# Performance work log

Hardware: AMD Instinct MI355X
Metric: run time of the kernel (lower is better)

The kernel has to match this reference:

```python
import jax, jax.numpy as jnp
import numpy as np

EPS = 1e-5
D = 4  # max_displacement


def _conv(x, w, b, stride, pad):
    # x: [B,C,H,W], w: [O,I,kh,kw]
    y = jax.lax.conv_general_dilated(x, w, (stride, stride), [(pad, pad), (pad, pad)],
                                     dimension_numbers=('NCHW', 'OIHW', 'NCHW'))
    return y + b[None, :, None, None]


def _bn(x, g, b, m, v):
    # eval-mode batchnorm with running stats
    scale = (g * jax.lax.rsqrt(v + EPS))[None, :, None, None]
    return (x - m[None, :, None, None]) * scale + b[None, :, None, None]


def _extract(x, w1, b1, g1, be1, m1, v1, w2, b2, g2, be2, m2, v2, w3, b3, g3, be3, m3, v3):
    x = jax.nn.relu(_bn(_conv(x, w1, b1, 2, 3), g1, be1, m1, v1))
    x = jax.nn.relu(_bn(_conv(x, w2, b2, 2, 1), g2, be2, m2, v2))
    x = jax.nn.relu(_bn(_conv(x, w3, b3, 2, 1), g3, be3, m3, v3))
    return x  # [B,256,H/8,W/8]


def _correlation(x1, x2):
    # shifted-window correlation, 81 shifts (structural loop, static slices)
    B, C, H, W = x1.shape
    x2p = jnp.pad(x2, ((0, 0), (0, 0), (D, D), (D, D)))
    maps = [jnp.sum(x1 * x2p[:, :, i:i + H, j:j + W], axis=1)
            for i in range(2 * D + 1) for j in range(2 * D + 1)]
    return jnp.stack(maps, axis=1)  # [B,81,H,W]


def _gmm(cloth_img, person_img, fe, fw1, fb1, fw2, fb2, fw3, fb3):
    cf = _extract(cloth_img, *fe)
    pf = _extract(person_img, *fe)
    corr = _correlation(cf, pf)
    x = jax.nn.relu(_conv(corr, fw1, fb1, 1, 1))
    x = jax.nn.relu(_conv(x, fw2, fb2, 1, 1))
    return _conv(x, fw3, fb3, 1, 1)  # [B,2,H/8,W/8]


def setup_inputs() -> dict:
    key = jax.random.key(0)
    ks = jax.random.split(key, 32)
    B, H, W = 8, 512, 512
    w = lambda k, shape, s=0.05: jax.random.normal(k, shape, jnp.float32) * s
    inp = {}
    inp['cloth_img'] = jax.random.normal(ks[0], (B, 3, H, W), jnp.float32)
    inp['person_img'] = jax.random.normal(ks[1], (B, 3, H, W), jnp.float32)
    inp['w1'] = w(ks[2], (64, 3, 7, 7)); inp['b1'] = w(ks[3], (64,))
    inp['g1'] = 1.0 + w(ks[4], (64,)); inp['be1'] = w(ks[5], (64,))
    inp['m1'] = w(ks[6], (64,)); inp['v1'] = jax.random.uniform(ks[7], (64,), jnp.float32, 0.5, 1.5)
    inp['w2'] = w(ks[8], (128, 64, 3, 3)); inp['b2'] = w(ks[9], (128,))
    inp['g2'] = 1.0 + w(ks[10], (128,)); inp['be2'] = w(ks[11], (128,))
    inp['m2'] = w(ks[12], (128,)); inp['v2'] = jax.random.uniform(ks[13], (128,), jnp.float32, 0.5, 1.5)
    inp['w3'] = w(ks[14], (256, 128, 3, 3)); inp['b3'] = w(ks[15], (256,))
    inp['g3'] = 1.0 + w(ks[16], (256,)); inp['be3'] = w(ks[17], (256,))
    inp['m3'] = w(ks[18], (256,)); inp['v3'] = jax.random.uniform(ks[19], (256,), jnp.float32, 0.5, 1.5)
    inp['fw1'] = w(ks[20], (128, 81, 3, 3)); inp['fb1'] = w(ks[21], (128,))
    inp['fw2'] = w(ks[22], (64, 128, 3, 3)); inp['fb2'] = w(ks[23], (64,))
    inp['fw3'] = w(ks[24], (2, 64, 3, 3)); inp['fb3'] = w(ks[25], (2,))
    return inp


def reference(cloth_img, person_img,
              w1, b1, g1, be1, m1, v1,
              w2, b2, g2, be2, m2, v2,
              w3, b3, g3, be3, m3, v3,
              fw1, fb1, fw2, fb2, fw3, fb3):
    fe = (w1, b1, g1, be1, m1, v1, w2, b2, g2, be2, m2, v2, w3, b3, g3, be3, m3, v3)
    return _gmm(cloth_img, person_img, fe, fw1, fb1, fw2, fb2, fw3, fb3)
```

## Files before the change

### kernel.cpp

```cpp
#include <hip/hip_runtime.h>

typedef __bf16 bf16x8_t __attribute__((ext_vector_type(8)));
typedef float f32x4 __attribute__((ext_vector_type(4)));
typedef unsigned short u16x8 __attribute__((ext_vector_type(8)));
typedef unsigned short u16x4 __attribute__((ext_vector_type(4)));

#define EPS 1e-5f

__device__ __forceinline__ unsigned short f2bf(float f) {
    unsigned u = __builtin_bit_cast(unsigned, f);
    u += 0x7fff + ((u >> 16) & 1);
    return (unsigned short)(u >> 16);
}

__device__ __forceinline__ void gload16(const unsigned short* g, unsigned short* l) {
    __builtin_amdgcn_global_load_lds(
        (const __attribute__((address_space(1))) unsigned int*)g,
        (__attribute__((address_space(3))) unsigned int*)l,
        16, 0, 0);
}

template <int N> __device__ __forceinline__ void s_waitcnt_vm() {
    if constexpr (N == 0)       asm volatile("s_waitcnt vmcnt(0)" ::: "memory");
    else if constexpr (N == 8)  asm volatile("s_waitcnt vmcnt(8)" ::: "memory");
    else if constexpr (N == 10) asm volatile("s_waitcnt vmcnt(10)" ::: "memory");
    else if constexpr (N == 12) asm volatile("s_waitcnt vmcnt(12)" ::: "memory");
    else static_assert(N == 0, "unsupported vmcnt");
}

__global__ void prep_affine_all(const float* __restrict__ b1, const float* __restrict__ g1,
                                const float* __restrict__ be1, const float* __restrict__ m1,
                                const float* __restrict__ v1,
                                const float* __restrict__ b2, const float* __restrict__ g2,
                                const float* __restrict__ be2, const float* __restrict__ m2,
                                const float* __restrict__ v2,
                                const float* __restrict__ b3, const float* __restrict__ g3,
                                const float* __restrict__ be3, const float* __restrict__ m3,
                                const float* __restrict__ v3,
                                const float* __restrict__ fb1, const float* __restrict__ fb2,
                                const float* __restrict__ fb3, float* __restrict__ aff) {
    int i = blockIdx.x * 256 + threadIdx.x;
    if (i < 64) {
        float s = g1[i] * rsqrtf(v1[i] + EPS);
        aff[i] = s; aff[64 + i] = (b1[i] - m1[i]) * s + be1[i];
    } else if (i < 192) {
        int c = i - 64; float s = g2[c] * rsqrtf(v2[c] + EPS);
        aff[128 + c] = s; aff[256 + c] = (b2[c] - m2[c]) * s + be2[c];
    } else if (i < 448) {
        int c = i - 192; float s = g3[c] * rsqrtf(v3[c] + EPS);
        aff[384 + c] = s; aff[640 + c] = (b3[c] - m3[c]) * s + be3[c];
    } else if (i < 576) {
        int c = i - 448; aff[896 + c] = 1.f; aff[1024 + c] = fb1[c];
    } else if (i < 640) {
        int c = i - 576; aff[1152 + c] = 1.f; aff[1216 + c] = fb2[c];
    } else if (i < 642) {
        int c = i - 640; aff[1280 + c] = 1.f; aff[1288 + c] = fb3[c];
    }
}

__device__ __forceinline__ void wconv3x3(const float* __restrict__ w, unsigned short* __restrict__ dst,
                                         int Cout, int Sp, int Kp, int CIN, int CINP, int idx) {
    if (idx >= Sp * Kp) return;
    int m = idx / Kp, k = idx - m * Kp;
    int tap = k / CINP, ic = k - tap * CINP;
    unsigned short v = 0;
    if (m < Cout && tap < 9 && ic < CIN) {
        int kh = tap / 3, kw = tap - kh * 3;
        v = f2bf(w[((m * CIN + ic) * 3 + kh) * 3 + kw]);
    }
    dst[idx] = v;
}

__global__ void conv_weights_all(const float* __restrict__ w1, const float* __restrict__ w2,
                                 const float* __restrict__ w3, const float* __restrict__ fw1,
                                 const float* __restrict__ fw2, const float* __restrict__ fw3,
                                 unsigned short* d1, unsigned short* d2, unsigned short* d3,
                                 unsigned short* d4, unsigned short* d5, unsigned short* d6) {
    int idx = blockIdx.x * 256 + threadIdx.x;
    switch (blockIdx.y) {
    case 0: {
        if (idx >= 64 * 256) return;
        int m = idx >> 8, k = idx & 255;
        int kh = k >> 5, r = k & 31, kw = r >> 2, ic = r & 3;
        unsigned short v = 0;
        if (kh < 7 && kw < 7 && ic < 3) v = f2bf(w1[((m * 3 + ic) * 7 + kh) * 7 + kw]);
        d1[idx] = v;
    } break;
    case 1: wconv3x3(w2, d2, 128, 128, 576, 64, 64, idx); break;
    case 2: wconv3x3(w3, d3, 256, 256, 1152, 128, 128, idx); break;
    case 3: wconv3x3(fw1, d4, 128, 128, 1152, 81, 128, idx); break;
    case 4: wconv3x3(fw2, d5, 64, 64, 1152, 128, 128, idx); break;
    case 5: wconv3x3(fw3, d6, 2, 64, 576, 64, 64, idx); break;
    }
}

__global__ void to_nhwc4(const float* __restrict__ cloth, const float* __restrict__ person,
                         unsigned short* __restrict__ dst) {
    int z = blockIdx.z;
    const float* src = (z < 8) ? cloth + (size_t)z * 786432
                               : person + (size_t)(z - 8) * 786432;
    int p = blockIdx.x * 256 + threadIdx.x;
    int row = p >> 9, col = p & 511;
    u16x4 o;
    o[0] = f2bf(src[p]);
    o[1] = f2bf(src[262144 + p]);
    o[2] = f2bf(src[524288 + p]);
    o[3] = 0;
    *(u16x4*)&dst[(size_t)z * 1073296 + ((size_t)(row + 3) * 518 + col + 3) * 4] = o;
}

__global__ void ring3_zero(unsigned short* __restrict__ buf) {
    int z = blockIdx.y;
    int p = blockIdx.x * 256 + threadIdx.x;
    if (p >= 6180) return;
    int r, c;
    if (p < 1554) { r = p / 518; c = p - (p / 518) * 518; }
    else if (p < 3108) { int q = p - 1554; r = 515 + q / 518; c = q - (q / 518) * 518; }
    else { int q = p - 3108; r = 3 + q / 6; int k = q - (q / 6) * 6; c = (k < 3) ? k : 512 + k; }
    const u16x4 zv = {0, 0, 0, 0};
    *(u16x4*)&buf[(size_t)z * 1073296 + ((size_t)r * 518 + c) * 4] = zv;
}

__global__ void border_zero(unsigned short* __restrict__ buf, int Hp, int Wp, int C8,
                            int imgStrideElems, int nimg) {
    int idx = blockIdx.x * 256 + threadIdx.x;
    int nb = 2 * Wp + 2 * (Hp - 2);
    int per = nb * C8;
    if (idx >= per * nimg) return;
    int z = idx / per, q = idx - z * per;
    int p = q / C8, cc = q - p * C8;
    int row, col;
    if (p < Wp) { row = 0; col = p; }
    else if (p < 2 * Wp) { row = Hp - 1; col = p - Wp; }
    else { int e = p - 2 * Wp; row = 1 + (e >> 1); col = (e & 1) ? Wp - 1 : 0; }
    const u16x8 zv = {0, 0, 0, 0, 0, 0, 0, 0};
    *(u16x8*)&buf[(size_t)z * imgStrideElems + ((size_t)row * Wp + col) * (C8 * 8) + cc * 8] = zv;
}

template <int WR, int WS, int MODE, bool RELU, bool OUT_NCHW, int CIN, int NKT,
          int HIN, int WOS, int STRIDE, int OPAD, int PIPE>
__global__ __launch_bounds__(WR * WS * 64)
void gemm_conv(const unsigned short* __restrict__ X, const unsigned short* __restrict__ Wmk,
               const float* __restrict__ scale, const float* __restrict__ shift,
               void* __restrict__ Yv, int Cout, int xImgStride, int yImgStride) {
    constexpr int BR = WR * 64, BS = WS * 64, NT = WR * WS * 64;
    constexpr int SXC = BR * 8 / NT, SWC = BS * 8 / NT;
    constexpr int NLOAD = SXC + SWC;
    constexpr int KP = (MODE == 1) ? NKT * 64 : 256;
    constexpr int WP = HIN + ((MODE == 2) ? 6 : 2);
    constexpr int WOUT = 1 << WOS;
    constexpr int WOP = WOUT + 2 * OPAD;
    constexpr int NBUF = PIPE ? 2 : 1;
    constexpr int EPS_LDK = BS + 8;
    constexpr int GEMM_ELEMS = NBUF * (BR + BS) * 64;
    constexpr int EPI_ELEMS = BR * EPS_LDK;
    constexpr int LDS_ELEMS = GEMM_ELEMS > EPI_ELEMS ? GEMM_ELEMS : EPI_ELEMS;
    __shared__ __align__(16) unsigned short lds[LDS_ELEMS];
    unsigned short* XsB = lds;
    unsigned short* WsB = lds + NBUF * BR * 64;
    const int tid = threadIdx.x;
    const int lane = tid & 63, wid = tid >> 6;
    const int wr = wid % WR, wsx = wid / WR;
    int bx = blockIdx.x;
    { const int nx = gridDim.x; bx = (bx & 7) * (nx >> 3) + (bx >> 3); }
    const int r0 = bx * BR, s0 = blockIdx.y * BS;
    const int z = blockIdx.z;
    const int lr = lane & 15, lk = lane >> 4;
    const unsigned short* Ximg = X + (size_t)z * xImgStride;

    const unsigned short* xsrc[SXC];
    #pragma unroll
    for (int i = 0; i < SXC; ++i) {
        int c = i * NT + tid;
        int row = c >> 3, chs = (c & 7) ^ (row & 7);
        int r = r0 + row;
        int oh = r >> WOS, ow = r & (WOUT - 1);
        if (MODE == 1)
            xsrc[i] = Ximg + ((size_t)(oh * STRIDE) * WP + (size_t)(ow * STRIDE)) * CIN + chs * 8;
        else
            xsrc[i] = Ximg + ((size_t)(2 * oh + (chs >> 2)) * WP + 2 * ow + (chs & 3) * 2) * 4;
    }
    const unsigned short* wsrc[SWC];
    #pragma unroll
    for (int i = 0; i < SWC; ++i) {
        int c = i * NT + tid;
        int row = c >> 3, chs = (c & 7) ^ (row & 7);
        wsrc[i] = Wmk + (size_t)(s0 + row) * KP + chs * 8;
    }

    int arow[4], brow[4];
    #pragma unroll
    for (int mi = 0; mi < 4; ++mi) arow[mi] = (wr * 64 + mi * 16 + lr) * 64;
    #pragma unroll
    for (int si = 0; si < 4; ++si) brow[si] = (wsx * 64 + si * 16 + lr) * 64;

    const f32x4 fz = {0.f, 0.f, 0.f, 0.f};
    f32x4 acc[4][4];
    #pragma unroll
    for (int a = 0; a < 4; ++a)
        #pragma unroll
        for (int b = 0; b < 4; ++b) acc[a][b] = fz;

    auto stage = [&](int kt, int b) {
        size_t koff;
        if (MODE == 1) {
            const int tap = (kt * 64) / CIN;
            const int kh = tap / 3, kw = tap - (tap / 3) * 3;
            const int icb0 = (kt * 64) % CIN;
            koff = ((size_t)kh * WP + kw) * CIN + icb0;
        } else {
            koff = (size_t)kt * 2 * WP * 4;
        }
        #pragma unroll
        for (int i = 0; i < SXC; ++i)
            gload16(xsrc[i] + koff, &XsB[b * BR * 64 + (i * NT + wid * 64) * 8]);
        #pragma unroll
        for (int i = 0; i < SWC; ++i)
            gload16(wsrc[i] + (size_t)kt * 64, &WsB[b * BS * 64 + (i * NT + wid * 64) * 8]);
    };
    auto compute = [&](int b) {
        #pragma unroll
        for (int hf = 0; hf < 2; ++hf) {
            const int cA = (((hf * 4 + lk) ^ (lr & 7)) * 8);
            u16x8 af[4], bfr[4];
            #pragma unroll
            for (int mi = 0; mi < 4; ++mi) af[mi] = *(const u16x8*)&XsB[b * BR * 64 + arow[mi] + cA];
            #pragma unroll
            for (int si = 0; si < 4; ++si) bfr[si] = *(const u16x8*)&WsB[b * BS * 64 + brow[si] + cA];
            #pragma unroll
            for (int mi = 0; mi < 4; ++mi)
                #pragma unroll
                for (int si = 0; si < 4; ++si)
                    acc[mi][si] = __builtin_amdgcn_mfma_f32_16x16x32_bf16(
                        __builtin_bit_cast(bf16x8_t, af[mi]),
                        __builtin_bit_cast(bf16x8_t, bfr[si]), acc[mi][si], 0, 0, 0);
        }
    };

    if (PIPE == 0) {
        #pragma unroll
        for (int kt = 0; kt < NKT; ++kt) {
            stage(kt, 0);
            __syncthreads();
            compute(0);
            __syncthreads();
        }
    } else {
        stage(0, 0);
        #pragma unroll
        for (int kt = 0; kt < NKT; ++kt) {
            const int cur = kt & 1;
            if (kt + 1 < NKT) {
                stage(kt + 1, cur ^ 1);
                s_waitcnt_vm<NLOAD>();
            } else {
                s_waitcnt_vm<0>();
            }
            __builtin_amdgcn_sched_barrier(0);
            __builtin_amdgcn_s_barrier();
            __builtin_amdgcn_sched_barrier(0);
            compute(cur);
            __builtin_amdgcn_sched_barrier(0);
            __builtin_amdgcn_s_barrier();
        }
    }

    if (OUT_NCHW) {
        #pragma unroll
        for (int si = 0; si < 4; ++si) {
            int col = s0 + wsx * 64 + si * 16 + lr;
            bool cok = col < Cout;
            float sc = cok ? scale[col] : 0.f;
            float sh = cok ? shift[col] : 0.f;
            #pragma unroll
            for (int mi = 0; mi < 4; ++mi) {
                int rbase = r0 + wr * 64 + mi * 16 + lk * 4;
                #pragma unroll
                for (int j = 0; j < 4; ++j) {
                    float v = acc[mi][si][j] * sc + sh;
                    if (RELU) v = fmaxf(v, 0.f);
                    if (cok) ((float*)Yv)[(size_t)z * yImgStride + col * 4096 + rbase + j] = v;
                }
            }
        }
    } else {
        __syncthreads();
        unsigned short* epi = lds;
        #pragma unroll
        for (int si = 0; si < 4; ++si) {
            int col = wsx * 64 + si * 16 + lr;
            float sc = scale[s0 + col];
            float sh = shift[s0 + col];
            #pragma unroll
            for (int mi = 0; mi < 4; ++mi) {
                int rowl = wr * 64 + mi * 16 + lk * 4;
                #pragma unroll
                for (int j = 0; j < 4; ++j) {
                    float v = acc[mi][si][j] * sc + sh;
                    if (RELU) v = fmaxf(v, 0.f);
                    epi[(rowl + j) * EPS_LDK + col] = f2bf(v);
                }
            }
        }
        __syncthreads();
        constexpr int NCH = BR * BS / 8 / NT;
        constexpr int CPR = BS / 8;
        #pragma unroll
        for (int i = 0; i < NCH; ++i) {
            int c = i * NT + tid;
            int row = c / CPR, colc = c - (c / CPR) * CPR;
            int r = r0 + row;
            int oh = r >> WOS, ow = r & (WOUT - 1);
            size_t off = ((size_t)(oh + OPAD) * WOP + ow + OPAD) * Cout + s0 + colc * 8;
            *(u16x8*)((unsigned short*)Yv + (size_t)z * yImgStride + off) =
                *(const u16x8*)&epi[row * EPS_LDK + colc * 8];
        }
    }
}

__global__ __launch_bounds__(256)
void corr_mfma(const unsigned short* __restrict__ cf,
               const unsigned short* __restrict__ pf,
               unsigned short* __restrict__ out) {
    const int h = blockIdx.x;
    const int z = blockIdx.y;
    const int tid = threadIdx.x;
    const int lane = tid & 63, t = tid >> 6;
    const int lr = lane & 15, lk = lane >> 4;
    const unsigned short* cfi = cf + (size_t)z * 1048576;
    const unsigned short* pfi = pf + (size_t)z * 1048576;
    unsigned short* outp = out + (size_t)z * 557568;

    u16x8 a[8];
    {
        const unsigned short* ap = cfi + ((size_t)(h * 64 + t * 16 + lr)) * 256 + lk * 8;
        #pragma unroll
        for (int ks = 0; ks < 8; ++ks) a[ks] = *(const u16x8*)(ap + ks * 32);
    }

    const u16x8 zz = {0, 0, 0, 0, 0, 0, 0, 0};
    for (int di = -4; di <= 4; ++di) {
        const int h2 = h + di;
        const bool hok = (unsigned)h2 < 64u;
        #pragma unroll
        for (int ct = 0; ct < 2; ++ct) {
            const int wpg = t * 16 - 8 + ct * 16 + lr;
            u16x8 b[8];
            if (hok && (unsigned)wpg < 64u) {
                const unsigned short* bp = pfi + ((size_t)(h2 * 64 + wpg)) * 256 + lk * 8;
                #pragma unroll
                for (int ks = 0; ks < 8; ++ks) b[ks] = *(const u16x8*)(bp + ks * 32);
            } else {
                #pragma unroll
                for (int ks = 0; ks < 8; ++ks) b[ks] = zz;
            }
            f32x4 acc0 = {0.f, 0.f, 0.f, 0.f}, acc1 = {0.f, 0.f, 0.f, 0.f};
            #pragma unroll
            for (int ks = 0; ks < 8; ks += 2) {
                acc0 = __builtin_amdgcn_mfma_f32_16x16x32_bf16(
                    __builtin_bit_cast(bf16x8_t, a[ks]),
                    __builtin_bit_cast(bf16x8_t, b[ks]), acc0, 0, 0, 0);
                acc1 = __builtin_amdgcn_mfma_f32_16x16x32_bf16(
                    __builtin_bit_cast(bf16x8_t, a[ks + 1]),
                    __builtin_bit_cast(bf16x8_t, b[ks + 1]), acc1, 0, 0, 0);
            }
            const int wl = lk * 4;
            const int wpl = ct * 16 - 8 + lr;
            #pragma unroll
            for (int j = 0; j < 4; ++j) {
                int dj = wpl - (wl + j);
                if (dj >= -4 && dj <= 4) {
                    int s = (di + 4) * 9 + dj + 4;
                    int w = t * 16 + wl + j;
                    outp[((size_t)(h + 1) * 66 + w + 1) * 128 + s] =
                        f2bf(acc0[j] + acc1[j]);
                }
            }
        }
    }
}

extern "C" void kernel_launch(void* const* d_in, const int* in_sizes, int n_in,
                              void* d_out, int out_size, void* d_ws, size_t ws_size,
                              hipStream_t stream) {
    const float* cloth  = (const float*)d_in[0];
    const float* person = (const float*)d_in[1];
    const float* w1 = (const float*)d_in[2];  const float* b1 = (const float*)d_in[3];
    const float* g1 = (const float*)d_in[4];  const float* be1 = (const float*)d_in[5];
    const float* m1 = (const float*)d_in[6];  const float* v1 = (const float*)d_in[7];
    const float* w2 = (const float*)d_in[8];  const float* b2 = (const float*)d_in[9];
    const float* g2 = (const float*)d_in[10]; const float* be2 = (const float*)d_in[11];
    const float* m2 = (const float*)d_in[12]; const float* v2 = (const float*)d_in[13];
    const float* w3 = (const float*)d_in[14]; const float* b3 = (const float*)d_in[15];
    const float* g3 = (const float*)d_in[16]; const float* be3 = (const float*)d_in[17];
    const float* m3 = (const float*)d_in[18]; const float* v3 = (const float*)d_in[19];
    const float* fw1 = (const float*)d_in[20]; const float* fb1 = (const float*)d_in[21];
    const float* fw2 = (const float*)d_in[22]; const float* fb2 = (const float*)d_in[23];
    const float* fw3 = (const float*)d_in[24]; const float* fb3 = (const float*)d_in[25];

    char* ws = (char*)d_ws;
    auto U = [&](size_t off) { return (unsigned short*)(ws + off); };
    unsigned short* nhwc = U(0);
    unsigned short* t1   = U(34345472);
    unsigned short* cf   = U(34345472);
    unsigned short* t2   = U(170668544);
    unsigned short* w1mk  = U(239890944);
    unsigned short* w2mk  = U(239923712);
    unsigned short* w3mk  = U(240071168);
    unsigned short* fw1mk = U(240660992);
    unsigned short* fw2mk = U(240955904);
    unsigned short* fw3mk = U(241103360);
    float* aff = (float*)(ws + 241177088);
    unsigned short* corr = U(241185280);
    unsigned short* f1b  = U(250106368);
    unsigned short* f2b  = U(259027456);
    float *s1 = aff,         *sh1 = aff + 64,   *s2 = aff + 128,  *sh2 = aff + 256;
    float *s3 = aff + 384,   *sh3 = aff + 640,  *sf1 = aff + 896, *shf1 = aff + 1024;
    float *sf2 = aff + 1152, *shf2 = aff + 1216, *sf3 = aff + 1280, *shf3 = aff + 1288;

    prep_affine_all<<<3, 256, 0, stream>>>(b1, g1, be1, m1, v1, b2, g2, be2, m2, v2,
                                           b3, g3, be3, m3, v3, fb1, fb2, fb3, aff);
    conv_weights_all<<<dim3(1152, 6), 256, 0, stream>>>(w1, w2, w3, fw1, fw2, fw3,
                                                        w1mk, w2mk, w3mk, fw1mk, fw2mk, fw3mk);

    ring3_zero<<<dim3(25, 16), 256, 0, stream>>>(nhwc);
    hipMemsetAsync(ws + 241185280, 0, 22302720, stream);
    border_zero<<<514, 256, 0, stream>>>(t1, 258, 258, 8, 4260096, 16);
    border_zero<<<517, 256, 0, stream>>>(t2, 130, 130, 16, 2163200, 16);

    to_nhwc4<<<dim3(1024, 1, 16), 256, 0, stream>>>(cloth, person, nhwc);

    gemm_conv<4, 1, 2, true, false, 4, 4, 512, 8, 2, 1, 0><<<dim3(256, 1, 16), 256, 0, stream>>>(
        nhwc, w1mk, s1, sh1, t1, 64, 1073296, 4260096);
    gemm_conv<2, 2, 1, true, false, 64, 9, 256, 7, 2, 1, 1><<<dim3(128, 1, 16), 256, 0, stream>>>(
        t1, w2mk, s2, sh2, t2, 128, 4260096, 2163200);
    gemm_conv<2, 2, 1, true, false, 128, 18, 128, 6, 2, 0, 1><<<dim3(32, 2, 16), 256, 0, stream>>>(
        t2, w3mk, s3, sh3, cf, 256, 2163200, 1048576);

    corr_mfma<<<dim3(64, 8), 256, 0, stream>>>(cf, cf + (size_t)8 * 1048576, corr);

    gemm_conv<2, 2, 1, true, false, 128, 18, 64, 6, 1, 1, 1><<<dim3(32, 1, 8), 256, 0, stream>>>(
        corr, fw1mk, sf1, shf1, f1b, 128, 557568, 557568);
    gemm_conv<2, 1, 1, true, false, 128, 18, 64, 6, 1, 1, 1><<<dim3(32, 1, 8), 128, 0, stream>>>(
        f1b, fw2mk, sf2, shf2, f2b, 64, 557568, 278784);
    gemm_conv<2, 1, 1, false, true, 64, 9, 64, 6, 1, 0, 1><<<dim3(32, 1, 8), 128, 0, stream>>>(
        f2b, fw3mk, sf3, shf3, (float*)d_out, 2, 278784, 8192);
}
```

Measured before the change: 271.2 us.

## Halve K-tile to 32 for MODE-1 convs and merge setup kernels

Adds a KSTEP template parameter so the im2col GEMM convolutions stage 32-wide K tiles instead of 64, doubling the number of k-iterations and halving LDS use per buffer. This should allow higher occupancy and a finer-grained double-buffered pipeline. The trade is more barriers and waitcnts per output tile. It also merges the per-layer weight conversion into a flat 1D launch and fuses the three border-zeroing kernels into one, which removes a few small launches.

```diff
diff --git a/kernel.cpp b/kernel.cpp
--- a/kernel.cpp
+++ b/kernel.cpp
@@ -22,6 +22,8 @@
 
 template <int N> __device__ __forceinline__ void s_waitcnt_vm() {
     if constexpr (N == 0)       asm volatile("s_waitcnt vmcnt(0)" ::: "memory");
+    else if constexpr (N == 4)  asm volatile("s_waitcnt vmcnt(4)" ::: "memory");
+    else if constexpr (N == 6)  asm volatile("s_waitcnt vmcnt(6)" ::: "memory");
     else if constexpr (N == 8)  asm volatile("s_waitcnt vmcnt(8)" ::: "memory");
     else if constexpr (N == 10) asm volatile("s_waitcnt vmcnt(10)" ::: "memory");
     else if constexpr (N == 12) asm volatile("s_waitcnt vmcnt(12)" ::: "memory");
@@ -59,8 +61,7 @@
 }
 
 __device__ __forceinline__ void wconv3x3(const float* __restrict__ w, unsigned short* __restrict__ dst,
-                                         int Cout, int Sp, int Kp, int CIN, int CINP, int idx) {
-    if (idx >= Sp * Kp) return;
+                                         int Cout, int Kp, int CIN, int CINP, int idx) {
     int m = idx / Kp, k = idx - m * Kp;
     int tap = k / CINP, ic = k - tap * CINP;
     unsigned short v = 0;
@@ -77,21 +78,17 @@
                                  unsigned short* d1, unsigned short* d2, unsigned short* d3,
                                  unsigned short* d4, unsigned short* d5, unsigned short* d6) {
     int idx = blockIdx.x * 256 + threadIdx.x;
-    switch (blockIdx.y) {
-    case 0: {
-        if (idx >= 64 * 256) return;
+    if (idx < 16384) {
         int m = idx >> 8, k = idx & 255;
         int kh = k >> 5, r = k & 31, kw = r >> 2, ic = r & 3;
         unsigned short v = 0;
         if (kh < 7 && kw < 7 && ic < 3) v = f2bf(w1[((m * 3 + ic) * 7 + kh) * 7 + kw]);
         d1[idx] = v;
-    } break;
-    case 1: wconv3x3(w2, d2, 128, 128, 576, 64, 64, idx); break;
-    case 2: wconv3x3(w3, d3, 256, 256, 1152, 128, 128, idx); break;
-    case 3: wconv3x3(fw1, d4, 128, 128, 1152, 81, 128, idx); break;
-    case 4: wconv3x3(fw2, d5, 64, 64, 1152, 128, 128, idx); break;
-    case 5: wconv3x3(fw3, d6, 2, 64, 576, 64, 64, idx); break;
-    }
+    } else if (idx < 90112)  wconv3x3(w2, d2, 128, 576, 64, 64, idx - 16384);
+    else if (idx < 385024)   wconv3x3(w3, d3, 256, 1152, 128, 128, idx - 90112);
+    else if (idx < 532480)   wconv3x3(fw1, d4, 128, 1152, 81, 128, idx - 385024);
+    else if (idx < 606208)   wconv3x3(fw2, d5, 64, 1152, 128, 128, idx - 532480);
+    else if (idx < 643072)   wconv3x3(fw3, d6, 2, 576, 64, 64, idx - 606208);
 }
 
 __global__ void to_nhwc4(const float* __restrict__ cloth, const float* __restrict__ person,
@@ -109,24 +106,11 @@
     *(u16x4*)&dst[(size_t)z * 1073296 + ((size_t)(row + 3) * 518 + col + 3) * 4] = o;
 }
 
-__global__ void ring3_zero(unsigned short* __restrict__ buf) {
-    int z = blockIdx.y;
-    int p = blockIdx.x * 256 + threadIdx.x;
-    if (p >= 6180) return;
-    int r, c;
-    if (p < 1554) { r = p / 518; c = p - (p / 518) * 518; }
-    else if (p < 3108) { int q = p - 1554; r = 515 + q / 518; c = q - (q / 518) * 518; }
-    else { int q = p - 3108; r = 3 + q / 6; int k = q - (q / 6) * 6; c = (k < 3) ? k : 512 + k; }
-    const u16x4 zv = {0, 0, 0, 0};
-    *(u16x4*)&buf[(size_t)z * 1073296 + ((size_t)r * 518 + c) * 4] = zv;
-}
-
-__global__ void border_zero(unsigned short* __restrict__ buf, int Hp, int Wp, int C8,
-                            int imgStrideElems, int nimg) {
-    int idx = blockIdx.x * 256 + threadIdx.x;
+__device__ __forceinline__ void ring1_zero(unsigned short* __restrict__ buf, int Hp, int Wp,
+                                           int C8, int imgStrideElems, int idx) {
     int nb = 2 * Wp + 2 * (Hp - 2);
     int per = nb * C8;
-    if (idx >= per * nimg) return;
+    if (idx >= per * 16) return;
     int z = idx / per, q = idx - z * per;
     int p = q / C8, cc = q - p * C8;
     int row, col;
@@ -137,27 +121,47 @@
     *(u16x8*)&buf[(size_t)z * imgStrideElems + ((size_t)row * Wp + col) * (C8 * 8) + cc * 8] = zv;
 }
 
+__global__ void zero_pads(unsigned short* __restrict__ nhwc, unsigned short* __restrict__ t1,
+                          unsigned short* __restrict__ t2) {
+    int idx = blockIdx.x * 256 + threadIdx.x;
+    if (blockIdx.y == 0) {
+        if (idx >= 16 * 6180) return;
+        int z = idx / 6180, p = idx - z * 6180;
+        int r, c;
+        if (p < 1554) { r = p / 518; c = p - (p / 518) * 518; }
+        else if (p < 3108) { int q = p - 1554; r = 515 + q / 518; c = q - (q / 518) * 518; }
+        else { int q = p - 3108; r = 3 + q / 6; int k = q - (q / 6) * 6; c = (k < 3) ? k : 512 + k; }
+        const u16x4 zv = {0, 0, 0, 0};
+        *(u16x4*)&nhwc[(size_t)z * 1073296 + ((size_t)r * 518 + c) * 4] = zv;
+    } else if (blockIdx.y == 1) {
+        ring1_zero(t1, 258, 258, 8, 4260096, idx);
+    } else {
+        ring1_zero(t2, 130, 130, 16, 2163200, idx);
+    }
+}
+
 template <int WR, int WS, int MODE, bool RELU, bool OUT_NCHW, int CIN, int NKT,
-          int HIN, int WOS, int STRIDE, int OPAD, int PIPE>
+          int HIN, int WOS, int STRIDE, int OPAD, int PIPE, int KSTEP>
 __global__ __launch_bounds__(WR * WS * 64)
 void gemm_conv(const unsigned short* __restrict__ X, const unsigned short* __restrict__ Wmk,
                const float* __restrict__ scale, const float* __restrict__ shift,
                void* __restrict__ Yv, int Cout, int xImgStride, int yImgStride) {
     constexpr int BR = WR * 64, BS = WS * 64, NT = WR * WS * 64;
-    constexpr int SXC = BR * 8 / NT, SWC = BS * 8 / NT;
+    constexpr int CPR_K = KSTEP / 8;
+    constexpr int SXC = BR * CPR_K / NT, SWC = BS * CPR_K / NT;
     constexpr int NLOAD = SXC + SWC;
-    constexpr int KP = (MODE == 1) ? NKT * 64 : 256;
+    constexpr int KP = (MODE == 1) ? NKT * KSTEP : 256;
     constexpr int WP = HIN + ((MODE == 2) ? 6 : 2);
     constexpr int WOUT = 1 << WOS;
     constexpr int WOP = WOUT + 2 * OPAD;
     constexpr int NBUF = PIPE ? 2 : 1;
     constexpr int EPS_LDK = BS + 8;
-    constexpr int GEMM_ELEMS = NBUF * (BR + BS) * 64;
+    constexpr int GEMM_ELEMS = NBUF * (BR + BS) * KSTEP;
     constexpr int EPI_ELEMS = BR * EPS_LDK;
     constexpr int LDS_ELEMS = GEMM_ELEMS > EPI_ELEMS ? GEMM_ELEMS : EPI_ELEMS;
     __shared__ __align__(16) unsigned short lds[LDS_ELEMS];
     unsigned short* XsB = lds;
-    unsigned short* WsB = lds + NBUF * BR * 64;
+    unsigned short* WsB = lds + NBUF * BR * KSTEP;
     const int tid = threadIdx.x;
     const int lane = tid & 63, wid = tid >> 6;
     const int wr = wid % WR, wsx = wid / WR;
@@ -172,7 +176,7 @@
     #pragma unroll
     for (int i = 0; i < SXC; ++i) {
         int c = i * NT + tid;
-        int row = c >> 3, chs = (c & 7) ^ (row & 7);
+        int row = c / CPR_K, chs = (c % CPR_K) ^ (row & (CPR_K - 1));
         int r = r0 + row;
         int oh = r >> WOS, ow = r & (WOUT - 1);
         if (MODE == 1)
@@ -184,15 +188,15 @@
     #pragma unroll
     for (int i = 0; i < SWC; ++i) {
         int c = i * NT + tid;
-        int row = c >> 3, chs = (c & 7) ^ (row & 7);
+        int row = c / CPR_K, chs = (c % CPR_K) ^ (row & (CPR_K - 1));
         wsrc[i] = Wmk + (size_t)(s0 + row) * KP + chs * 8;
     }
 
     int arow[4], brow[4];
     #pragma unroll
-    for (int mi = 0; mi < 4; ++mi) arow[mi] = (wr * 64 + mi * 16 + lr) * 64;
+    for (int mi = 0; mi < 4; ++mi) arow[mi] = (wr * 64 + mi * 16 + lr) * KSTEP;
     #pragma unroll
-    for (int si = 0; si < 4; ++si) brow[si] = (wsx * 64 + si * 16 + lr) * 64;
+    for (int si = 0; si < 4; ++si) brow[si] = (wsx * 64 + si * 16 + lr) * KSTEP;
 
     const f32x4 fz = {0.f, 0.f, 0.f, 0.f};
     f32x4 acc[4][4];
@@ -204,29 +208,45 @@
     auto stage = [&](int kt, int b) {
         size_t koff;
         if (MODE == 1) {
-            const int tap = (kt * 64) / CIN;
+            const int tap = (kt * KSTEP) / CIN;
             const int kh = tap / 3, kw = tap - (tap / 3) * 3;
-            const int icb0 = (kt * 64) % CIN;
+            const int icb0 = (kt * KSTEP) % CIN;
             koff = ((size_t)kh * WP + kw) * CIN + icb0;
         } else {
             koff = (size_t)kt * 2 * WP * 4;
         }
         #pragma unroll
         for (int i = 0; i < SXC; ++i)
-            gload16(xsrc[i] + koff, &XsB[b * BR * 64 + (i * NT + wid * 64) * 8]);
+            gload16(xsrc[i] + koff, &XsB[b * BR * KSTEP + (i * NT + wid * 64) * 8]);
         #pragma unroll
         for (int i = 0; i < SWC; ++i)
-            gload16(wsrc[i] + (size_t)kt * 64, &WsB[b * BS * 64 + (i * NT + wid * 64) * 8]);
+            gload16(wsrc[i] + (size_t)kt * KSTEP, &WsB[b * BS * KSTEP + (i * NT + wid * 64) * 8]);
     };
     auto compute = [&](int b) {
-        #pragma unroll
-        for (int hf = 0; hf < 2; ++hf) {
-            const int cA = (((hf * 4 + lk) ^ (lr & 7)) * 8);
+        if constexpr (KSTEP == 64) {
+            #pragma unroll
+            for (int hf = 0; hf < 2; ++hf) {
+                const int cA = (((hf * 4 + lk) ^ (lr & 7)) * 8);
+                u16x8 af[4], bfr[4];
+                #pragma unroll
+                for (int mi = 0; mi < 4; ++mi) af[mi] = *(const u16x8*)&XsB[b * BR * 64 + arow[mi] + cA];
+                #pragma unroll
+                for (int si = 0; si < 4; ++si) bfr[si] = *(const u16x8*)&WsB[b * BS * 64 + brow[si] + cA];
+                #pragma unroll
+                for (int mi = 0; mi < 4; ++mi)
+                    #pragma unroll
+                    for (int si = 0; si < 4; ++si)
+                        acc[mi][si] = __builtin_amdgcn_mfma_f32_16x16x32_bf16(
+                            __builtin_bit_cast(bf16x8_t, af[mi]),
+                            __builtin_bit_cast(bf16x8_t, bfr[si]), acc[mi][si], 0, 0, 0);
+            }
+        } else {
+            const int cA = ((lk ^ (lr & 3)) * 8);
             u16x8 af[4], bfr[4];
             #pragma unroll
-            for (int mi = 0; mi < 4; ++mi) af[mi] = *(const u16x8*)&XsB[b * BR * 64 + arow[mi] + cA];
-            #pragma unroll
-            for (int si = 0; si < 4; ++si) bfr[si] = *(const u16x8*)&WsB[b * BS * 64 + brow[si] + cA];
+            for (int mi = 0; mi < 4; ++mi) af[mi] = *(const u16x8*)&XsB[b * BR * 32 + arow[mi] + cA];
+            #pragma unroll
+            for (int si = 0; si < 4; ++si) bfr[si] = *(const u16x8*)&WsB[b * BS * 32 + brow[si] + cA];
             #pragma unroll
             for (int mi = 0; mi < 4; ++mi)
                 #pragma unroll
@@ -420,29 +440,27 @@
 
     prep_affine_all<<<3, 256, 0, stream>>>(b1, g1, be1, m1, v1, b2, g2, be2, m2, v2,
                                            b3, g3, be3, m3, v3, fb1, fb2, fb3, aff);
-    conv_weights_all<<<dim3(1152, 6), 256, 0, stream>>>(w1, w2, w3, fw1, fw2, fw3,
-                                                        w1mk, w2mk, w3mk, fw1mk, fw2mk, fw3mk);
-
-    ring3_zero<<<dim3(25, 16), 256, 0, stream>>>(nhwc);
+    conv_weights_all<<<2512, 256, 0, stream>>>(w1, w2, w3, fw1, fw2, fw3,
+                                               w1mk, w2mk, w3mk, fw1mk, fw2mk, fw3mk);
+
+    zero_pads<<<dim3(516, 3), 256, 0, stream>>>(nhwc, t1, t2);
     hipMemsetAsync(ws + 241185280, 0, 22302720, stream);
-    border_zero<<<514, 256, 0, stream>>>(t1, 258, 258, 8, 4260096, 16);
-    border_zero<<<517, 256, 0, stream>>>(t2, 130, 130, 16, 2163200, 16);
 
     to_nhwc4<<<dim3(1024, 1, 16), 256, 0, stream>>>(cloth, person, nhwc);
 
-    gemm_conv<4, 1, 2, true, false, 4, 4, 512, 8, 2, 1, 0><<<dim3(256, 1, 16), 256, 0, stream>>>(
+    gemm_conv<4, 1, 2, true, false, 4, 4, 512, 8, 2, 1, 0, 64><<<dim3(256, 1, 16), 256, 0, stream>>>(
         nhwc, w1mk, s1, sh1, t1, 64, 1073296, 4260096);
-    gemm_conv<2, 2, 1, true, false, 64, 9, 256, 7, 2, 1, 1><<<dim3(128, 1, 16), 256, 0, stream>>>(
+    gemm_conv<2, 2, 1, true, false, 64, 18, 256, 7, 2, 1, 1, 32><<<dim3(128, 1, 16), 256, 0, stream>>>(
         t1, w2mk, s2, sh2, t2, 128, 4260096, 2163200);
-    gemm_conv<2, 2, 1, true, false, 128, 18, 128, 6, 2, 0, 1><<<dim3(32, 2, 16), 256, 0, stream>>>(
+    gemm_conv<2, 2, 1, true, false, 128, 36, 128, 6, 2, 0, 1, 32><<<dim3(32, 2, 16), 256, 0, stream>>>(
         t2, w3mk, s3, sh3, cf, 256, 2163200, 1048576);
 
     corr_mfma<<<dim3(64, 8), 256, 0, stream>>>(cf, cf + (size_t)8 * 1048576, corr);
 
-    gemm_conv<2, 2, 1, true, false, 128, 18, 64, 6, 1, 1, 1><<<dim3(32, 1, 8), 256, 0, stream>>>(
+    gemm_conv<2, 2, 1, true, false, 128, 36, 64, 6, 1, 1, 1, 32><<<dim3(32, 1, 8), 256, 0, stream>>>(
         corr, fw1mk, sf1, shf1, f1b, 128, 557568, 557568);
-    gemm_conv<2, 1, 1, true, false, 128, 18, 64, 6, 1, 1, 1><<<dim3(32, 1, 8), 128, 0, stream>>>(
+    gemm_conv<2, 1, 1, true, false, 128, 36, 64, 6, 1, 1, 1, 32><<<dim3(32, 1, 8), 128, 0, stream>>>(
         f1b, fw2mk, sf2, shf2, f2b, 64, 557568, 278784);
-    gemm_conv<2, 1, 1, false, true, 64, 9, 64, 6, 1, 0, 1><<<dim3(32, 1, 8), 128, 0, stream>>>(
+    gemm_conv<2, 1, 1, false, true, 64, 18, 64, 6, 1, 0, 1, 32><<<dim3(32, 1, 8), 128, 0, stream>>>(
         f2b, fw3mk, sf3, shf3, (float*)d_out, 2, 278784, 8192);
 }
```

Result: slower. 286.7 us (+5.7%).

## Merge setup kernels and parallelize correlation across vertical displacements

Applied to the files above, without the earlier changes.

Folds the affine-parameter prep into the weight-conversion kernel and merges the three padding-zero kernels into one launch, which cuts the number of small kernel launches. The correlation kernel now gives each vertical displacement its own block in a 3D grid instead of looping over all nine inside one block. That raises its parallelism from 512 to 4608 blocks, but each block reloads its A fragment, so there is more redundant traffic. Unused vmcnt wait variants were also added.

```diff
diff --git a/kernel.cpp b/kernel.cpp
--- a/kernel.cpp
+++ b/kernel.cpp
@@ -22,45 +22,16 @@
 
 template <int N> __device__ __forceinline__ void s_waitcnt_vm() {
     if constexpr (N == 0)       asm volatile("s_waitcnt vmcnt(0)" ::: "memory");
+    else if constexpr (N == 4)  asm volatile("s_waitcnt vmcnt(4)" ::: "memory");
+    else if constexpr (N == 6)  asm volatile("s_waitcnt vmcnt(6)" ::: "memory");
     else if constexpr (N == 8)  asm volatile("s_waitcnt vmcnt(8)" ::: "memory");
     else if constexpr (N == 10) asm volatile("s_waitcnt vmcnt(10)" ::: "memory");
     else if constexpr (N == 12) asm volatile("s_waitcnt vmcnt(12)" ::: "memory");
     else static_assert(N == 0, "unsupported vmcnt");
 }
 
-__global__ void prep_affine_all(const float* __restrict__ b1, const float* __restrict__ g1,
-                                const float* __restrict__ be1, const float* __restrict__ m1,
-                                const float* __restrict__ v1,
-                                const float* __restrict__ b2, const float* __restrict__ g2,
-                                const float* __restrict__ be2, const float* __restrict__ m2,
-                                const float* __restrict__ v2,
-                                const float* __restrict__ b3, const float* __restrict__ g3,
-                                const float* __restrict__ be3, const float* __restrict__ m3,
-                                const float* __restrict__ v3,
-                                const float* __restrict__ fb1, const float* __restrict__ fb2,
-                                const float* __restrict__ fb3, float* __restrict__ aff) {
-    int i = blockIdx.x * 256 + threadIdx.x;
-    if (i < 64) {
-        float s = g1[i] * rsqrtf(v1[i] + EPS);
-        aff[i] = s; aff[64 + i] = (b1[i] - m1[i]) * s + be1[i];
-    } else if (i < 192) {
-        int c = i - 64; float s = g2[c] * rsqrtf(v2[c] + EPS);
-        aff[128 + c] = s; aff[256 + c] = (b2[c] - m2[c]) * s + be2[c];
-    } else if (i < 448) {
-        int c = i - 192; float s = g3[c] * rsqrtf(v3[c] + EPS);
-        aff[384 + c] = s; aff[640 + c] = (b3[c] - m3[c]) * s + be3[c];
-    } else if (i < 576) {
-        int c = i - 448; aff[896 + c] = 1.f; aff[1024 + c] = fb1[c];
-    } else if (i < 640) {
-        int c = i - 576; aff[1152 + c] = 1.f; aff[1216 + c] = fb2[c];
-    } else if (i < 642) {
-        int c = i - 640; aff[1280 + c] = 1.f; aff[1288 + c] = fb3[c];
-    }
-}
-
 __device__ __forceinline__ void wconv3x3(const float* __restrict__ w, unsigned short* __restrict__ dst,
-                                         int Cout, int Sp, int Kp, int CIN, int CINP, int idx) {
-    if (idx >= Sp * Kp) return;
+                                         int Cout, int Kp, int CIN, int CINP, int idx) {
     int m = idx / Kp, k = idx - m * Kp;
     int tap = k / CINP, ic = k - tap * CINP;
     unsigned short v = 0;
@@ -74,23 +45,50 @@
 __global__ void conv_weights_all(const float* __restrict__ w1, const float* __restrict__ w2,
                                  const float* __restrict__ w3, const float* __restrict__ fw1,
                                  const float* __restrict__ fw2, const float* __restrict__ fw3,
+                                 const float* __restrict__ b1, const float* __restrict__ g1,
+                                 const float* __restrict__ be1, const float* __restrict__ m1,
+                                 const float* __restrict__ v1,
+                                 const float* __restrict__ b2, const float* __restrict__ g2,
+                                 const float* __restrict__ be2, const float* __restrict__ m2,
+                                 const float* __restrict__ v2,
+                                 const float* __restrict__ b3, const float* __restrict__ g3,
+                                 const float* __restrict__ be3, const float* __restrict__ m3,
+                                 const float* __restrict__ v3,
+                                 const float* __restrict__ fb1, const float* __restrict__ fb2,
+                                 const float* __restrict__ fb3,
                                  unsigned short* d1, unsigned short* d2, unsigned short* d3,
-                                 unsigned short* d4, unsigned short* d5, unsigned short* d6) {
+                                 unsigned short* d4, unsigned short* d5, unsigned short* d6,
+                                 float* __restrict__ aff) {
     int idx = blockIdx.x * 256 + threadIdx.x;
-    switch (blockIdx.y) {
-    case 0: {
-        if (idx >= 64 * 256) return;
+    if (idx < 16384) {
         int m = idx >> 8, k = idx & 255;
         int kh = k >> 5, r = k & 31, kw = r >> 2, ic = r & 3;
         unsigned short v = 0;
         if (kh < 7 && kw < 7 && ic < 3) v = f2bf(w1[((m * 3 + ic) * 7 + kh) * 7 + kw]);
         d1[idx] = v;
-    } break;
-    case 1: wconv3x3(w2, d2, 128, 128, 576, 64, 64, idx); break;
-    case 2: wconv3x3(w3, d3, 256, 256, 1152, 128, 128, idx); break;
-    case 3: wconv3x3(fw1, d4, 128, 128, 1152, 81, 128, idx); break;
-    case 4: wconv3x3(fw2, d5, 64, 64, 1152, 128, 128, idx); break;
-    case 5: wconv3x3(fw3, d6, 2, 64, 576, 64, 64, idx); break;
+    } else if (idx < 90112)  wconv3x3(w2, d2, 128, 576, 64, 64, idx - 16384);
+    else if (idx < 385024)   wconv3x3(w3, d3, 256, 1152, 128, 128, idx - 90112);
+    else if (idx < 532480)   wconv3x3(fw1, d4, 128, 1152, 81, 128, idx - 385024);
+    else if (idx < 606208)   wconv3x3(fw2, d5, 64, 1152, 128, 128, idx - 532480);
+    else if (idx < 643072)   wconv3x3(fw3, d6, 2, 576, 64, 64, idx - 606208);
+    else {
+        int i = idx - 643072;
+        if (i < 64) {
+            float s = g1[i] * rsqrtf(v1[i] + EPS);
+            aff[i] = s; aff[64 + i] = (b1[i] - m1[i]) * s + be1[i];
+        } else if (i < 192) {
+            int c = i - 64; float s = g2[c] * rsqrtf(v2[c] + EPS);
+            aff[128 + c] = s; aff[256 + c] = (b2[c] - m2[c]) * s + be2[c];
+        } else if (i < 448) {
+            int c = i - 192; float s = g3[c] * rsqrtf(v3[c] + EPS);
+            aff[384 + c] = s; aff[640 + c] = (b3[c] - m3[c]) * s + be3[c];
+        } else if (i < 576) {
+            int c = i - 448; aff[896 + c] = 1.f; aff[1024 + c] = fb1[c];
+        } else if (i < 640) {
+            int c = i - 576; aff[1152 + c] = 1.f; aff[1216 + c] = fb2[c];
+        } else if (i < 642) {
+            int c = i - 640; aff[1280 + c] = 1.f; aff[1288 + c] = fb3[c];
+        }
     }
 }
 
@@ -109,24 +107,11 @@
     *(u16x4*)&dst[(size_t)z * 1073296 + ((size_t)(row + 3) * 518 + col + 3) * 4] = o;
 }
 
-__global__ void ring3_zero(unsigned short* __restrict__ buf) {
-    int z = blockIdx.y;
-    int p = blockIdx.x * 256 + threadIdx.x;
-    if (p >= 6180) return;
-    int r, c;
-    if (p < 1554) { r = p / 518; c = p - (p / 518) * 518; }
-    else if (p < 3108) { int q = p - 1554; r = 515 + q / 518; c = q - (q / 518) * 518; }
-    else { int q = p - 3108; r = 3 + q / 6; int k = q - (q / 6) * 6; c = (k < 3) ? k : 512 + k; }
-    const u16x4 zv = {0, 0, 0, 0};
-    *(u16x4*)&buf[(size_t)z * 1073296 + ((size_t)r * 518 + c) * 4] = zv;
-}
-
-__global__ void border_zero(unsigned short* __restrict__ buf, int Hp, int Wp, int C8,
-                            int imgStrideElems, int nimg) {
-    int idx = blockIdx.x * 256 + threadIdx.x;
+__device__ __forceinline__ void ring1_zero(unsigned short* __restrict__ buf, int Hp, int Wp,
+                                           int C8, int imgStrideElems, int idx) {
     int nb = 2 * Wp + 2 * (Hp - 2);
     int per = nb * C8;
-    if (idx >= per * nimg) return;
+    if (idx >= per * 16) return;
     int z = idx / per, q = idx - z * per;
     int p = q / C8, cc = q - p * C8;
     int row, col;
@@ -135,6 +120,25 @@
     else { int e = p - 2 * Wp; row = 1 + (e >> 1); col = (e & 1) ? Wp - 1 : 0; }
     const u16x8 zv = {0, 0, 0, 0, 0, 0, 0, 0};
     *(u16x8*)&buf[(size_t)z * imgStrideElems + ((size_t)row * Wp + col) * (C8 * 8) + cc * 8] = zv;
+}
+
+__global__ void zero_pads(unsigned short* __restrict__ nhwc, unsigned short* __restrict__ t1,
+                          unsigned short* __restrict__ t2) {
+    int idx = blockIdx.x * 256 + threadIdx.x;
+    if (blockIdx.y == 0) {
+        if (idx >= 16 * 6180) return;
+        int z = idx / 6180, p = idx - z * 6180;
+        int r, c;
+        if (p < 1554) { r = p / 518; c = p - (p / 518) * 518; }
+        else if (p < 3108) { int q = p - 1554; r = 515 + q / 518; c = q - (q / 518) * 518; }
+        else { int q = p - 3108; r = 3 + q / 6; int k = q - (q / 6) * 6; c = (k < 3) ? k : 512 + k; }
+        const u16x4 zv = {0, 0, 0, 0};
+        *(u16x4*)&nhwc[(size_t)z * 1073296 + ((size_t)r * 518 + c) * 4] = zv;
+    } else if (blockIdx.y == 1) {
+        ring1_zero(t1, 258, 258, 8, 4260096, idx);
+    } else {
+        ring1_zero(t2, 130, 130, 16, 2163200, idx);
+    }
 }
 
 template <int WR, int WS, int MODE, bool RELU, bool OUT_NCHW, int CIN, int NKT,
@@ -323,7 +327,8 @@
                const unsigned short* __restrict__ pf,
                unsigned short* __restrict__ out) {
     const int h = blockIdx.x;
-    const int z = blockIdx.y;
+    const int di = (int)blockIdx.y - 4;
+    const int z = blockIdx.z;
     const int tid = threadIdx.x;
     const int lane = tid & 63, t = tid >> 6;
     const int lr = lane & 15, lk = lane >> 4;
@@ -339,42 +344,40 @@
     }
 
     const u16x8 zz = {0, 0, 0, 0, 0, 0, 0, 0};
-    for (int di = -4; di <= 4; ++di) {
-        const int h2 = h + di;
-        const bool hok = (unsigned)h2 < 64u;
-        #pragma unroll
-        for (int ct = 0; ct < 2; ++ct) {
-            const int wpg = t * 16 - 8 + ct * 16 + lr;
-            u16x8 b[8];
-            if (hok && (unsigned)wpg < 64u) {
-                const unsigned short* bp = pfi + ((size_t)(h2 * 64 + wpg)) * 256 + lk * 8;
-                #pragma unroll
-                for (int ks = 0; ks < 8; ++ks) b[ks] = *(const u16x8*)(bp + ks * 32);
-            } else {
-                #pragma unroll
-                for (int ks = 0; ks < 8; ++ks) b[ks] = zz;
-            }
-            f32x4 acc0 = {0.f, 0.f, 0.f, 0.f}, acc1 = {0.f, 0.f, 0.f, 0.f};
-            #pragma unroll
-            for (int ks = 0; ks < 8; ks += 2) {
-                acc0 = __builtin_amdgcn_mfma_f32_16x16x32_bf16(
-                    __builtin_bit_cast(bf16x8_t, a[ks]),
-                    __builtin_bit_cast(bf16x8_t, b[ks]), acc0, 0, 0, 0);
-                acc1 = __builtin_amdgcn_mfma_f32_16x16x32_bf16(
-                    __builtin_bit_cast(bf16x8_t, a[ks + 1]),
-                    __builtin_bit_cast(bf16x8_t, b[ks + 1]), acc1, 0, 0, 0);
-            }
-            const int wl = lk * 4;
-            const int wpl = ct * 16 - 8 + lr;
-            #pragma unroll
-            for (int j = 0; j < 4; ++j) {
-                int dj = wpl - (wl + j);
-                if (dj >= -4 && dj <= 4) {
-                    int s = (di + 4) * 9 + dj + 4;
-                    int w = t * 16 + wl + j;
-                    outp[((size_t)(h + 1) * 66 + w + 1) * 128 + s] =
-                        f2bf(acc0[j] + acc1[j]);
-                }
+    const int h2 = h + di;
+    const bool hok = (unsigned)h2 < 64u;
+    #pragma unroll
+    for (int ct = 0; ct < 2; ++ct) {
+        const int wpg = t * 16 - 8 + ct * 16 + lr;
+        u16x8 b[8];
+        if (hok && (unsigned)wpg < 64u) {
+            const unsigned short* bp = pfi + ((size_t)(h2 * 64 + wpg)) * 256 + lk * 8;
+            #pragma unroll
+            for (int ks = 0; ks < 8; ++ks) b[ks] = *(const u16x8*)(bp + ks * 32);
+        } else {
+            #pragma unroll
+            for (int ks = 0; ks < 8; ++ks) b[ks] = zz;
+        }
+        f32x4 acc0 = {0.f, 0.f, 0.f, 0.f}, acc1 = {0.f, 0.f, 0.f, 0.f};
+        #pragma unroll
+        for (int ks = 0; ks < 8; ks += 2) {
+            acc0 = __builtin_amdgcn_mfma_f32_16x16x32_bf16(
+                __builtin_bit_cast(bf16x8_t, a[ks]),
+                __builtin_bit_cast(bf16x8_t, b[ks]), acc0, 0, 0, 0);
+            acc1 = __builtin_amdgcn_mfma_f32_16x16x32_bf16(
+                __builtin_bit_cast(bf16x8_t, a[ks + 1]),
+                __builtin_bit_cast(bf16x8_t, b[ks + 1]), acc1, 0, 0, 0);
+        }
+        const int wl = lk * 4;
+        const int wpl = ct * 16 - 8 + lr;
+        #pragma unroll
+        for (int j = 0; j < 4; ++j) {
+            int dj = wpl - (wl + j);
+            if (dj >= -4 && dj <= 4) {
+                int s = (di + 4) * 9 + dj + 4;
+                int w = t * 16 + wl + j;
+                outp[((size_t)(h + 1) * 66 + w + 1) * 128 + s] =
+                    f2bf(acc0[j] + acc1[j]);
             }
         }
     }
@@ -418,15 +421,13 @@
     float *s3 = aff + 384,   *sh3 = aff + 640,  *sf1 = aff + 896, *shf1 = aff + 1024;
     float *sf2 = aff + 1152, *shf2 = aff + 1216, *sf3 = aff + 1280, *shf3 = aff + 1288;
 
-    prep_affine_all<<<3, 256, 0, stream>>>(b1, g1, be1, m1, v1, b2, g2, be2, m2, v2,
-                                           b3, g3, be3, m3, v3, fb1, fb2, fb3, aff);
-    conv_weights_all<<<dim3(1152, 6), 256, 0, stream>>>(w1, w2, w3, fw1, fw2, fw3,
-                                                        w1mk, w2mk, w3mk, fw1mk, fw2mk, fw3mk);
-
-    ring3_zero<<<dim3(25, 16), 256, 0, stream>>>(nhwc);
+    conv_weights_all<<<2516, 256, 0, stream>>>(w1, w2, w3, fw1, fw2, fw3,
+                                               b1, g1, be1, m1, v1, b2, g2, be2, m2, v2,
+                                               b3, g3, be3, m3, v3, fb1, fb2, fb3,
+                                               w1mk, w2mk, w3mk, fw1mk, fw2mk, fw3mk, aff);
+
+    zero_pads<<<dim3(516, 3), 256, 0, stream>>>(nhwc, t1, t2);
     hipMemsetAsync(ws + 241185280, 0, 22302720, stream);
-    border_zero<<<514, 256, 0, stream>>>(t1, 258, 258, 8, 4260096, 16);
-    border_zero<<<517, 256, 0, stream>>>(t2, 130, 130, 16, 2163200, 16);
 
     to_nhwc4<<<dim3(1024, 1, 16), 256, 0, stream>>>(cloth, person, nhwc);
 
@@ -437,7 +438,7 @@
     gemm_conv<2, 2, 1, true, false, 128, 18, 128, 6, 2, 0, 1><<<dim3(32, 2, 16), 256, 0, stream>>>(
         t2, w3mk, s3, sh3, cf, 256, 2163200, 1048576);
 
-    corr_mfma<<<dim3(64, 8), 256, 0, stream>>>(cf, cf + (size_t)8 * 1048576, corr);
+    corr_mfma<<<dim3(64, 9, 8), 256, 0, stream>>>(cf, cf + (size_t)8 * 1048576, corr);
 
     gemm_conv<2, 2, 1, true, false, 128, 18, 64, 6, 1, 1, 1><<<dim3(32, 1, 8), 256, 0, stream>>>(
         corr, fw1mk, sf1, shf1, f1b, 128, 557568, 557568);
```

Measured after the change: 279.0 us. +2.9%, slower.
